# Optimization experiments

Hardware: AMD Instinct MI355X
Metric: run time of the kernel (lower is better)

The kernel has to match this reference:

```python
import jax, jax.numpy as jnp
import numpy as np
from jax import lax


def conv2d(x, w, b=None, pad=1):
    y = lax.conv_general_dilated(x, w, (1, 1), [(pad, pad), (pad, pad)],
                                 dimension_numbers=('NCHW', 'OIHW', 'NCHW'))
    return y if b is None else y + b[None, :, None, None]


def conv3d(x, w, b=None, pad=(0, 0, 0), dil=(1, 1, 1), groups=1):
    y = lax.conv_general_dilated(x, w, (1, 1, 1), [(p, p) for p in pad],
                                 rhs_dilation=dil,
                                 dimension_numbers=('NCDHW', 'OIDHW', 'NCDHW'),
                                 feature_group_count=groups)
    return y if b is None else y + b[None, :, None, None, None]


def base_grid(H, W, dtype):
    # normalized grid, channel 0 = x in [-1,1], channel 1 = y in [-1,1]
    gxn = 2.0 * jnp.arange(W, dtype=dtype) / max(W - 1, 1) - 1.0
    gyn = 2.0 * jnp.arange(H, dtype=dtype) / max(H - 1, 1) - 1.0
    return jnp.stack([jnp.broadcast_to(gxn[None, :], (H, W)),
                      jnp.broadcast_to(gyn[:, None], (H, W))], 0)


def grid_sample(img, grid):
    # img (N,C,H,W), grid (N,H,W,2) in [-1,1] (x,y); bilinear, zeros padding, align_corners=False
    N, C, H, W = img.shape
    gx = ((grid[..., 0] + 1.0) * W - 1.0) * 0.5
    gy = ((grid[..., 1] + 1.0) * H - 1.0) * 0.5
    x0 = jnp.floor(gx)
    y0 = jnp.floor(gy)
    wx = gx - x0
    wy = gy - y0

    def one(im, x0b, y0b, wxb, wyb):
        x0i = x0b.astype(jnp.int32)
        y0i = y0b.astype(jnp.int32)

        def samp(xi, yi):
            valid = (xi >= 0) & (xi < W) & (yi >= 0) & (yi < H)
            v = im[:, jnp.clip(yi, 0, H - 1), jnp.clip(xi, 0, W - 1)]
            return v * valid[None].astype(im.dtype)

        v00 = samp(x0i, y0i)
        v01 = samp(x0i + 1, y0i)
        v10 = samp(x0i, y0i + 1)
        v11 = samp(x0i + 1, y0i + 1)
        return (v00 * (1 - wxb) * (1 - wyb) + v01 * wxb * (1 - wyb)
                + v10 * (1 - wxb) * wyb + v11 * wxb * wyb)

    return jax.vmap(one)(img, x0, y0, wx, wy)


def ms_def_corr(x, y, off):
    # deformable correlation: per scale, warp y by that scale's offset and take
    # the channel-mean dot product with x -> (BT, S, H, W)
    BT, C, H, W = x.shape
    base = base_grid(H, W, x.dtype)
    sc = jnp.array([W - 1, H - 1], x.dtype)[None, :, None, None]
    S = off.shape[1] // 2
    corrs = []
    for i in range(S):
        vg = base[None] + off[:, 2 * i:2 * i + 2] / sc
        w = grid_sample(y, vg.transpose(0, 2, 3, 1))
        corrs.append(jnp.mean(x * w, axis=1))
    return jnp.stack(corrs, 1)


def corr_filter(corr, w1, w2):
    avg = jnp.mean(corr, 1, keepdims=True)
    mx = jnp.max(corr, 1, keepdims=True)
    var = jnp.var(corr, axis=1, keepdims=True, ddof=1)  # torch.var unbiased
    attn = jax.nn.sigmoid(conv2d(jnp.concatenate([avg, mx], 1), w1) + conv2d(var, w2))
    return corr * attn


def setup_inputs() -> dict:
    key = jax.random.key(0)
    ks = jax.random.split(key, 16)
    B, C, T, H, W = 2, 64, 16, 64, 64
    S = 3
    r = C // 16

    def n(k, shape, s=0.02):
        return jax.random.normal(k, shape, jnp.float32) * s

    return {
        'x': jax.random.normal(ks[0], (B, C, T, H, W), jnp.float32),
        'ofs_l_w1': n(ks[1], (C, 2 * C, 3, 3)), 'ofs_l_b1': jnp.zeros((C,), jnp.float32),
        'ofs_l_w2': n(ks[2], (2 * S, C, 3, 3)), 'ofs_l_b2': jnp.zeros((2 * S,), jnp.float32),
        'ofs_r_w1': n(ks[3], (C, 2 * C, 3, 3)), 'ofs_r_b1': jnp.zeros((C,), jnp.float32),
        'ofs_r_w2': n(ks[4], (2 * S, C, 3, 3)), 'ofs_r_b2': jnp.zeros((2 * S,), jnp.float32),
        'cf_w1': n(ks[5], (1, 2, 3, 3), 0.1), 'cf_w2': n(ks[6], (1, 1, 3, 3), 0.1),
        'down_w': n(ks[7], (r, C, 1, 1, 1), 0.1),
        'sa1_w': n(ks[8], (r, 1, 9, 3, 3), 0.1), 'sa1_b': jnp.zeros((r,), jnp.float32),
        'sa2_w': n(ks[9], (r, 1, 9, 3, 3), 0.1), 'sa2_b': jnp.zeros((r,), jnp.float32),
        'sa3_w': n(ks[10], (r, 1, 9, 3, 3), 0.1), 'sa3_b': jnp.zeros((r,), jnp.float32),
        'agg_w': jnp.ones((3,), jnp.float32) / 3,
        'back_w': n(ks[11], (C, r, 1, 1, 1), 0.1),
        'fusion_w': jnp.ones((2,), jnp.float32) / 2,
    }


def reference(x, ofs_l_w1, ofs_l_b1, ofs_l_w2, ofs_l_b2,
              ofs_r_w1, ofs_r_b1, ofs_r_w2, ofs_r_b2,
              cf_w1, cf_w2, down_w,
              sa1_w, sa1_b, sa2_w, sa2_b, sa3_w, sa3_b,
              agg_w, back_w, fusion_w):
    B, C, T, H, W = x.shape
    r = down_w.shape[0]

    # long-term branch: 1x1x1 down conv -> 3 dilated depthwise 3D convs -> 1x1x1 up conv
    x_agg = conv3d(x, down_w)
    agg = (conv3d(x_agg, sa1_w, sa1_b, (4, 1, 1), (1, 1, 1), r) * agg_w[0]
           + conv3d(x_agg, sa2_w, sa2_b, (4, 2, 2), (1, 2, 2), r) * agg_w[1]
           + conv3d(x_agg, sa3_w, sa3_b, (4, 3, 3), (1, 3, 3), r) * agg_w[2])
    long_term = jax.nn.sigmoid(conv3d(agg, back_w)) - 0.5

    # temporal shifts
    left = jnp.concatenate([x[:, :, 1:], x[:, :, -1:]], 2)
    right = jnp.concatenate([x[:, :, :1], x[:, :, :-1]], 2)
    xf = x.transpose(0, 2, 1, 3, 4).reshape(B * T, C, H, W)
    lf = left.transpose(0, 2, 1, 3, 4).reshape(B * T, C, H, W)
    rf = right.transpose(0, 2, 1, 3, 4).reshape(B * T, C, H, W)

    off_lm = conv2d(jax.nn.relu(conv2d(jnp.concatenate([xf, lf], 1), ofs_l_w1, ofs_l_b1)),
                    ofs_l_w2, ofs_l_b2)
    off_rm = conv2d(jax.nn.relu(conv2d(jnp.concatenate([xf, rf], 1), ofs_r_w1, ofs_r_b1)),
                    ofs_r_w2, ofs_r_b2)

    corr_lm = ms_def_corr(xf, lf, off_lm)
    corr_rm = ms_def_corr(xf, rf, off_rm)
    fcl = corr_filter(corr_lm, cf_w1, cf_w2)
    fcr = corr_filter(corr_rm, cf_w1, cf_w2)

    base = base_grid(H, W, x.dtype)
    sc = jnp.array([W - 1, H - 1], x.dtype)[None, :, None, None]
    vg_lm = base[None] + off_lm[:, :2] / sc
    vg_rm = base[None] + off_rm[:, :2] / sc
    warped_lm = grid_sample(lf, vg_lm.transpose(0, 2, 3, 1))
    warped_rm = grid_sample(rf, vg_rm.transpose(0, 2, 3, 1))

    attn_lm = jnp.mean(fcl, 1, keepdims=True)
    attn_rm = jnp.mean(fcr, 1, keepdims=True)
    feat_lm = warped_lm * (jax.nn.sigmoid(attn_lm) - 0.5)
    feat_rm = warped_rm * (jax.nn.sigmoid(attn_rm) - 0.5)

    short = fusion_w[0] * feat_lm + fusion_w[1] * feat_rm
    short = short.reshape(B, T, C, H, W).transpose(0, 2, 1, 3, 4)
    return short * long_term
```

## Files before the change

### kernel.cpp

```cpp
#include <hip/hip_runtime.h>
#include <hip/hip_bf16.h>
#include <math.h>


typedef __attribute__((ext_vector_type(8))) short short8v;
typedef __attribute__((ext_vector_type(4))) float f32x4;

#define HID_ELEMS 8650752ULL

__device__ __forceinline__ float sigmoidf_(float v) {
    return 1.0f / (1.0f + expf(-v));
}

__device__ __forceinline__ float bf2f(short s) {
    union { unsigned u; float f; } z;
    z.u = ((unsigned)(unsigned short)s) << 16;
    return z.f;
}

__device__ __forceinline__ void gll16(const __hip_bfloat16* g, __hip_bfloat16* l) {
    __builtin_amdgcn_global_load_lds((const __attribute__((address_space(1))) unsigned int*)(const void*)g,
                                     (__attribute__((address_space(3))) unsigned int*)(void*)l,
                                     16, 0, 0);
}

struct Samp { int o0, o1, o2, o3; float w0, w1, w2, w3; };

__device__ __forceinline__ Samp make_samp(float ox, float oy, int w, int h) {
    float bx = (2.0f * (float)w) / 63.0f - 1.0f;
    float by = (2.0f * (float)h) / 63.0f - 1.0f;
    float vx = bx + ox / 63.0f;
    float vy = by + oy / 63.0f;
    float gx = ((vx + 1.0f) * 64.0f - 1.0f) * 0.5f;
    float gy = ((vy + 1.0f) * 64.0f - 1.0f) * 0.5f;
    float fx = floorf(gx), fy = floorf(gy);
    float wx = gx - fx, wy = gy - fy;
    int x0 = (int)fx, y0 = (int)fy;
    int x1 = x0 + 1, y1 = y0 + 1;
    bool vx0 = (x0 >= 0) && (x0 < 64), vx1 = (x1 >= 0) && (x1 < 64);
    bool vy0 = (y0 >= 0) && (y0 < 64), vy1 = (y1 >= 0) && (y1 < 64);
    int cx0 = min(max(x0, 0), 63), cx1 = min(max(x1, 0), 63);
    int cy0 = min(max(y0, 0), 63), cy1 = min(max(y1, 0), 63);
    Samp s;
    s.o0 = cy0 * 4224 + (cx0 + 1) * 64; s.w0 = (1.0f - wx) * (1.0f - wy) * ((vx0 && vy0) ? 1.0f : 0.0f);
    s.o1 = cy0 * 4224 + (cx1 + 1) * 64; s.w1 = wx * (1.0f - wy) * ((vx1 && vy0) ? 1.0f : 0.0f);
    s.o2 = cy1 * 4224 + (cx0 + 1) * 64; s.w2 = (1.0f - wx) * wy * ((vx0 && vy1) ? 1.0f : 0.0f);
    s.o3 = cy1 * 4224 + (cx1 + 1) * 64; s.w3 = wx * wy * ((vx1 && vy1) ? 1.0f : 0.0f);
    return s;
}

__global__ __launch_bounds__(256) void k_prep_x(const float* __restrict__ x,
                                                const float* __restrict__ dw,
                                                __hip_bfloat16* __restrict__ xT,
                                                float* __restrict__ xa)
{
    int bid = blockIdx.x;
    int h = bid & 63;
    int n = bid >> 6;
    int b = n >> 4, t = n & 15;
    __shared__ float s[64][65];
    int tid = threadIdx.x;
    for (int idx = tid; idx < 4096; idx += 256) {
        int c = idx >> 6, w = idx & 63;
        s[c][w] = x[(((size_t)b * 64 + c) * 16 + t) * 4096 + h * 64 + w];
    }
    __syncthreads();
    __hip_bfloat16* op = xT + ((size_t)n * 64 + h) * 4224;
    for (int idx = tid; idx < 4224; idx += 256) {
        int wp = idx >> 6, c = idx & 63;
        float v = (wp == 0 || wp == 65) ? 0.f : s[c][wp - 1];
        op[idx] = __float2bfloat16(v);
    }
    int w = tid & 63, g = tid >> 6;
    float acc = 0.f;
    const float* dwg = dw + g * 64;
    #pragma unroll 8
    for (int c = 0; c < 64; c++) acc = fmaf(s[c][w], dwg[c], acc);
    xa[((size_t)(b * 4 + g) * 16 + t) * 4096 + h * 64 + w] = acc;
}

__global__ __launch_bounds__(256) void k_prep_w(const float* __restrict__ wl1,
                                                const float* __restrict__ wr1,
                                                const float* __restrict__ wl2,
                                                const float* __restrict__ wr2,
                                                __hip_bfloat16* __restrict__ Wmisc)
{
    int idx = blockIdx.x * 256 + threadIdx.x;
    if (idx < 147456) {
        int side = (idx >= 73728) ? 1 : 0;
        int i = idx - side * 73728;
        int ci = i & 127;
        int co = (i >> 7) & 63;
        int tap = i >> 13;
        const float* w = side ? wr1 : wl1;
        float v = w[((size_t)co * 128 + ci) * 9 + tap];
        int pos = side * 73728 + tap * 8192 + co * 128 + (ci ^ ((co & 15) << 3));
        Wmisc[pos] = __float2bfloat16(v);
    } else if (idx < 151680) {
        Wmisc[idx] = __float2bfloat16(0.f);
    } else if (idx < 170112) {
        int i2 = idx - 151680;
        int side = i2 / 9216;
        int j = i2 - side * 9216;
        int tap = j >> 10;
        int rem = j & 1023;
        int co = rem >> 6;
        int ci = rem & 63;
        const float* w = side ? wr2 : wl2;
        float v = (co < 6) ? w[((size_t)co * 64 + ci) * 9 + tap] : 0.f;
        Wmisc[idx] = __float2bfloat16(v);
    }
}

__global__ __launch_bounds__(512, 4) void k_conv1_mfma(const __hip_bfloat16* __restrict__ xT,
                                                       const __hip_bfloat16* __restrict__ Wb,
                                                       const __hip_bfloat16* __restrict__ zrow,
                                                       const float* __restrict__ b1l,
                                                       const float* __restrict__ b1r,
                                                       __hip_bfloat16* __restrict__ hidden,
                                                       int side_base, size_t hid_stride)
{
    __shared__ __hip_bfloat16 sB[24576];

    int bid = blockIdx.x;
    int side = side_base + (bid >> 9);
    int bid2 = bid & 511;
    int rq = bid2 & 15;
    int n = bid2 >> 4;
    int b = n >> 4, t = n & 15;
    int t2 = side ? max(t - 1, 0) : min(t + 1, 15);
    int n2 = b * 16 + t2;

    const __hip_bfloat16* WbS = Wb + (size_t)side * 73728;
    const float* b1 = side ? b1r : b1l;
    __hip_bfloat16* hs = hidden + (size_t)side * hid_stride;

    int tid = threadIdx.x;
    int wv = tid >> 6;
    int lane = tid & 63;
    int r = rq * 4 + (wv & 3);
    int m0 = (wv >> 2) * 32;
    int lr = lane & 15;
    int q = lane >> 4;
    int lk = q << 3;

    const __hip_bfloat16* fA0 = xT + (size_t)n * 270336;
    const __hip_bfloat16* fA1 = xT + (size_t)n2 * 270336;

    f32x4 acc[2][4];
    #pragma unroll
    for (int ni = 0; ni < 4; ni++) {
        float bb = b1[ni * 16 + lr];
        acc[0][ni] = (f32x4){bb, bb, bb, bb};
        acc[1][ni] = (f32x4){bb, bb, bb, bb};
    }

    int kx[2][2];
    #pragma unroll
    for (int khalf = 0; khalf < 2; khalf++)
        #pragma unroll
        for (int ks = 0; ks < 2; ks++)
            kx[khalf][ks] = ((khalf << 7) + (ks << 6) + (q << 4)) ^ (lr << 4);

    const char* sbc = (const char*)&sB[0];

    #pragma unroll
    for (int g = 0; g < 3; g++) {
        __syncthreads();
        {
            const __hip_bfloat16* wsrc = WbS + (size_t)g * 24576 + wv * 3072 + lane * 8;
            #pragma unroll
            for (int j = 0; j < 6; j++)
                gll16(wsrc + j * 512, &sB[wv * 3072 + j * 512]);
        }
        __syncthreads();

        int rr = r + g - 1;
        bool ok = (rr >= 0) && (rr < 64);
        const __hip_bfloat16* r0 = ok ? (fA0 + rr * 4224) : zrow;
        const __hip_bfloat16* r1 = ok ? (fA1 + rr * 4224) : zrow;

        #pragma unroll
        for (int tl = 0; tl < 3; tl++) {
            int abase = (m0 + lr + tl) * 64 + lk;
            #pragma unroll
            for (int khalf = 0; khalf < 2; khalf++) {
                const __hip_bfloat16* ar = khalf ? r1 : r0;
                short8v a00 = *(const short8v*)(ar + abase);
                short8v a01 = *(const short8v*)(ar + abase + 32);
                short8v a10 = *(const short8v*)(ar + abase + 1024);
                short8v a11 = *(const short8v*)(ar + abase + 1056);
                #pragma unroll
                for (int ni = 0; ni < 4; ni++) {
                    int rowb = tl * 16384 + ni * 4096 + lr * 256;
                    short8v b0  = *(const short8v*)(sbc + (rowb + kx[khalf][0]));
                    short8v b1v = *(const short8v*)(sbc + (rowb + kx[khalf][1]));
                    acc[0][ni] = __builtin_amdgcn_mfma_f32_16x16x32_bf16(a00, b0, acc[0][ni], 0, 0, 0);
                    acc[1][ni] = __builtin_amdgcn_mfma_f32_16x16x32_bf16(a10, b0, acc[1][ni], 0, 0, 0);
                    acc[0][ni] = __builtin_amdgcn_mfma_f32_16x16x32_bf16(a01, b1v, acc[0][ni], 0, 0, 0);
                    acc[1][ni] = __builtin_amdgcn_mfma_f32_16x16x32_bf16(a11, b1v, acc[1][ni], 0, 0, 0);
                }
            }
        }
    }

    int pxq = q << 2;
    __hip_bfloat16* hb = hs + (size_t)(n * 64 + r) * 4224;
    #pragma unroll
    for (int mi = 0; mi < 2; mi++) {
        #pragma unroll
        for (int ni = 0; ni < 4; ni++) {
            int co = ni * 16 + lr;
            #pragma unroll
            for (int j = 0; j < 4; j++) {
                int px = m0 + mi * 16 + pxq + j;
                float v = acc[mi][ni][j];
                v = v < 0.f ? 0.f : v;
                hb[(size_t)(px + 1) * 64 + co] = __float2bfloat16(v);
            }
        }
    }
    {
        int row_l = tid >> 7;
        int sel = (tid >> 6) & 1;
        int co = tid & 63;
        hs[(size_t)(n * 64 + rq * 4 + row_l) * 4224 + (sel ? 65 : 0) * 64 + co] = __float2bfloat16(0.f);
    }
}

__global__ __launch_bounds__(256) void k_conv2_mfma(const __hip_bfloat16* __restrict__ hidden,
                                                    const __hip_bfloat16* __restrict__ W2b,
                                                    const __hip_bfloat16* __restrict__ zrow,
                                                    const float* __restrict__ b2l,
                                                    const float* __restrict__ b2r,
                                                    float* __restrict__ off,
                                                    int side_base, size_t hid_stride)
{
    int bid = blockIdx.x;
    int side = side_base + (bid >> 9);
    int bid2 = bid & 511;
    int rq = bid2 & 15;
    int n = bid2 >> 4;
    int tid = threadIdx.x;
    int wv = tid >> 6;
    int lane = tid & 63;
    int r = rq * 4 + wv;
    int lr = lane & 15;
    int lk = (lane >> 4) << 3;

    const __hip_bfloat16* W2bS = W2b + (size_t)side * 9216;
    const float* b2 = side ? b2r : b2l;
    float* offS = off + (size_t)side * 786432;
    const __hip_bfloat16* hbase = hidden + (size_t)side * hid_stride + (size_t)n * 270336;

    float bb = (lr < 6) ? b2[lr] : 0.f;
    f32x4 acc[4];
    #pragma unroll
    for (int mi = 0; mi < 4; mi++) acc[mi] = (f32x4){bb, bb, bb, bb};

    #pragma unroll
    for (int tap = 0; tap < 9; tap++) {
        const int kh = tap / 3, kw = tap - (tap / 3) * 3;
        int rr = r + kh - 1;
        bool ok = (rr >= 0) && (rr < 64);
        const __hip_bfloat16* hr = ok ? (hbase + (size_t)rr * 4224) : zrow;
        const __hip_bfloat16* bw = W2bS + ((size_t)tap * 16 + lr) * 64 + lk;
        short8v b0 = *(const short8v*)(bw);
        short8v b1v = *(const short8v*)(bw + 32);
        #pragma unroll
        for (int mi = 0; mi < 4; mi++) {
            int abase = (mi * 16 + lr + kw) * 64 + lk;
            short8v a0 = *(const short8v*)(hr + abase);
            short8v a1 = *(const short8v*)(hr + abase + 32);
            acc[mi] = __builtin_amdgcn_mfma_f32_16x16x32_bf16(a0, b0, acc[mi], 0, 0, 0);
            acc[mi] = __builtin_amdgcn_mfma_f32_16x16x32_bf16(a1, b1v, acc[mi], 0, 0, 0);
        }
    }
    if (lr < 6) {
        int pxq = (lane >> 4) << 2;
        #pragma unroll
        for (int mi = 0; mi < 4; mi++) {
            #pragma unroll
            for (int j = 0; j < 4; j++) {
                int px = mi * 16 + pxq + j;
                offS[((size_t)n * 6 + lr) * 4096 + r * 64 + px] = acc[mi][j];
            }
        }
    }
}

__global__ __launch_bounds__(256) void k_agg(const float* __restrict__ xa,
                                             const float* __restrict__ w1, const float* __restrict__ b1,
                                             const float* __restrict__ w2, const float* __restrict__ b2,
                                             const float* __restrict__ w3, const float* __restrict__ b3,
                                             const float* __restrict__ aw,
                                             float* __restrict__ agg)
{
    int gid = blockIdx.x * 256 + threadIdx.x;
    int hw = gid & 4095;
    int rest = gid >> 12;
    int t = rest & 15;
    int g = (rest >> 4) & 3;
    int b = rest >> 6;
    int h = hw >> 6, w = hw & 63;
    const float* base = xa + ((size_t)(b * 4 + g) * 16) * 4096;
    const float* ws0 = w1 + g * 81;
    const float* ws1 = w2 + g * 81;
    const float* ws2 = w3 + g * 81;
    float acc0 = b1[g], acc1 = b2[g], acc2 = b3[g];
    for (int kd = 0; kd < 9; kd++) {
        int d = t + kd - 4;
        if (d < 0 || d > 15) continue;
        const float* fr = base + (size_t)d * 4096;
        #pragma unroll
        for (int kh = 0; kh < 3; kh++) {
            #pragma unroll
            for (int kw = 0; kw < 3; kw++) {
                int widx = kd * 9 + kh * 3 + kw;
                {
                    int yy = h + (kh - 1), xx = w + (kw - 1);
                    if (yy >= 0 && yy < 64 && xx >= 0 && xx < 64)
                        acc0 = fmaf(fr[yy * 64 + xx], ws0[widx], acc0);
                }
                {
                    int yy = h + (kh - 1) * 2, xx = w + (kw - 1) * 2;
                    if (yy >= 0 && yy < 64 && xx >= 0 && xx < 64)
                        acc1 = fmaf(fr[yy * 64 + xx], ws1[widx], acc1);
                }
                {
                    int yy = h + (kh - 1) * 3, xx = w + (kw - 1) * 3;
                    if (yy >= 0 && yy < 64 && xx >= 0 && xx < 64)
                        acc2 = fmaf(fr[yy * 64 + xx], ws2[widx], acc2);
                }
            }
        }
    }
    agg[gid] = acc0 * aw[0] + acc1 * aw[1] + acc2 * aw[2];
}

__global__ __launch_bounds__(256, 4) void k_corr2(const __hip_bfloat16* __restrict__ xT,
                                                  const float* __restrict__ off_l,
                                                  const float* __restrict__ off_r,
                                                  float* __restrict__ stats_l,
                                                  float* __restrict__ stats_r)
{
    int tid = threadIdx.x;
    int wv = tid >> 6;
    int lane = tid & 63;
    int pl = lane & 15;
    int cq = lane >> 4;
    int pidx = blockIdx.x * 64 + wv * 16 + pl;
    int half = pidx >> 17;
    int gid = pidx & 131071;
    const float* off = half ? off_r : off_l;
    float* stats = half ? stats_r : stats_l;

    int hw = gid & 4095;
    int n = gid >> 12;
    int b = n >> 4, t = n & 15;
    int t2 = half ? max(t - 1, 0) : min(t + 1, 15);
    int n2 = b * 16 + t2;
    int h = hw >> 6, w = hw & 63;
    int cc0 = cq * 16;

    const __hip_bfloat16* xf = xT + (size_t)n * 270336 + h * 4224 + (w + 1) * 64 + cc0;
    const __hip_bfloat16* yf = xT + (size_t)n2 * 270336 + cc0;

    Samp sp[3];
    #pragma unroll
    for (int s = 0; s < 3; s++) {
        float ox = off[((size_t)n * 6 + 2 * s) * 4096 + hw];
        float oy = off[((size_t)n * 6 + 2 * s + 1) * 4096 + hw];
        sp[s] = make_samp(ox, oy, w, h);
    }

    short8v xv0 = *(const short8v*)(xf);
    short8v xv1 = *(const short8v*)(xf + 8);

    int o0[4] = {sp[0].o0, sp[0].o1, sp[0].o2, sp[0].o3};
    int o1[4] = {sp[1].o0, sp[1].o1, sp[1].o2, sp[1].o3};
    int o2[4] = {sp[2].o0, sp[2].o1, sp[2].o2, sp[2].o3};

    short8v y0[4][2], y1[4][2], y2[4][2];
    #pragma unroll
    for (int cr = 0; cr < 4; cr++) {
        y0[cr][0] = *(const short8v*)(yf + o0[cr]);
        y0[cr][1] = *(const short8v*)(yf + o0[cr] + 8);
    }
    #pragma unroll
    for (int cr = 0; cr < 4; cr++) {
        y1[cr][0] = *(const short8v*)(yf + o1[cr]);
        y1[cr][1] = *(const short8v*)(yf + o1[cr] + 8);
    }

    float xs[16];
    #pragma unroll
    for (int e = 0; e < 8; e++) { xs[e] = bf2f(xv0[e]); xs[8 + e] = bf2f(xv1[e]); }

    float ac[3][4];
    #pragma unroll
    for (int s = 0; s < 3; s++)
        #pragma unroll
        for (int cr = 0; cr < 4; cr++) ac[s][cr] = 0.f;

    #pragma unroll
    for (int cr = 0; cr < 4; cr++)
        #pragma unroll
        for (int i = 0; i < 2; i++)
            #pragma unroll
            for (int e = 0; e < 8; e++)
                ac[0][cr] = fmaf(xs[i * 8 + e], bf2f(y0[cr][i][e]), ac[0][cr]);
    #pragma unroll
    for (int cr = 0; cr < 4; cr++) {
        y2[cr][0] = *(const short8v*)(yf + o2[cr]);
        y2[cr][1] = *(const short8v*)(yf + o2[cr] + 8);
    }
    #pragma unroll
    for (int cr = 0; cr < 4; cr++)
        #pragma unroll
        for (int i = 0; i < 2; i++)
            #pragma unroll
            for (int e = 0; e < 8; e++)
                ac[1][cr] = fmaf(xs[i * 8 + e], bf2f(y1[cr][i][e]), ac[1][cr]);
    #pragma unroll
    for (int cr = 0; cr < 4; cr++)
        #pragma unroll
        for (int i = 0; i < 2; i++)
            #pragma unroll
            for (int e = 0; e < 8; e++)
                ac[2][cr] = fmaf(xs[i * 8 + e], bf2f(y2[cr][i][e]), ac[2][cr]);

    #pragma unroll
    for (int s = 0; s < 3; s++)
        #pragma unroll
        for (int cr = 0; cr < 4; cr++) {
            float v = ac[s][cr];
            v += __shfl_xor(v, 16, 64);
            v += __shfl_xor(v, 32, 64);
            ac[s][cr] = v;
        }

    if (cq == 0) {
        float c[3];
        c[0] = (ac[0][0] * sp[0].w0 + ac[0][1] * sp[0].w1 + ac[0][2] * sp[0].w2 + ac[0][3] * sp[0].w3) * (1.0f / 64.0f);
        c[1] = (ac[1][0] * sp[1].w0 + ac[1][1] * sp[1].w1 + ac[1][2] * sp[1].w2 + ac[1][3] * sp[1].w3) * (1.0f / 64.0f);
        c[2] = (ac[2][0] * sp[2].w0 + ac[2][1] * sp[2].w1 + ac[2][2] * sp[2].w2 + ac[2][3] * sp[2].w3) * (1.0f / 64.0f);
        float avg = (c[0] + c[1] + c[2]) * (1.0f / 3.0f);
        float mx = fmaxf(c[0], fmaxf(c[1], c[2]));
        float d0 = c[0] - avg, d1 = c[1] - avg, d2 = c[2] - avg;
        float var = (d0 * d0 + d1 * d1 + d2 * d2) * 0.5f;
        stats[(size_t)n * 4096 + hw] = avg;
        stats[131072 + (size_t)n * 4096 + hw] = mx;
        stats[262144 + (size_t)n * 4096 + hw] = var;
    }
}

__device__ __forceinline__ float attn_val(const float* __restrict__ stats, int n, int hw,
                                          const float* __restrict__ cfw1,
                                          const float* __restrict__ cfw2)
{
    int h = hw >> 6, w = hw & 63;
    const float* avg = stats + (size_t)n * 4096;
    const float* mx  = stats + 131072 + (size_t)n * 4096;
    const float* var = stats + 262144 + (size_t)n * 4096;
    float s = 0.f;
    #pragma unroll
    for (int k = 0; k < 9; k++) {
        int kh = k / 3 - 1, kw = k - (k / 3) * 3 - 1;
        int yy = h + kh, xx = w + kw;
        if (yy >= 0 && yy < 64 && xx >= 0 && xx < 64) {
            int p = yy * 64 + xx;
            s += avg[p] * cfw1[k] + mx[p] * cfw1[9 + k] + var[p] * cfw2[k];
        }
    }
    float attn = sigmoidf_(s);
    return sigmoidf_(avg[hw] * attn) - 0.5f;
}

__global__ __launch_bounds__(256) void k_final(const __hip_bfloat16* __restrict__ xT,
                                               const float* __restrict__ off_l,
                                               const float* __restrict__ off_r,
                                               const float* __restrict__ stats_l,
                                               const float* __restrict__ stats_r,
                                               const float* __restrict__ cfw1,
                                               const float* __restrict__ cfw2,
                                               const float* __restrict__ agg,
                                               const float* __restrict__ backw,
                                               const float* __restrict__ fusw,
                                               float* __restrict__ out)
{
    int gid0 = blockIdx.x * 256 + threadIdx.x;
    int hw = gid0 & 4095;
    int ch = (gid0 >> 12) & 1;
    int n = gid0 >> 13;
    int b = n >> 4, t = n & 15;
    int tl = min(t + 1, 15), tr = max(t - 1, 0);
    int nl = b * 16 + tl, nr = b * 16 + tr;
    int h = hw >> 6, w = hw & 63;
    int cc0 = ch * 32;

    float oxl = off_l[((size_t)n * 6 + 0) * 4096 + hw];
    float oyl = off_l[((size_t)n * 6 + 1) * 4096 + hw];
    float oxr = off_r[((size_t)n * 6 + 0) * 4096 + hw];
    float oyr = off_r[((size_t)n * 6 + 1) * 4096 + hw];
    Samp sl = make_samp(oxl, oyl, w, h);
    Samp sr = make_samp(oxr, oyr, w, h);

    const __hip_bfloat16* lf = xT + (size_t)nl * 270336 + cc0;
    const __hip_bfloat16* rf = xT + (size_t)nr * 270336 + cc0;

    short8v lv[4][4], rv[4][4];
    #pragma unroll
    for (int i = 0; i < 4; i++) {
        lv[0][i] = *(const short8v*)(lf + sl.o0 + 8 * i);
        lv[1][i] = *(const short8v*)(lf + sl.o1 + 8 * i);
        lv[2][i] = *(const short8v*)(lf + sl.o2 + 8 * i);
        lv[3][i] = *(const short8v*)(lf + sl.o3 + 8 * i);
        rv[0][i] = *(const short8v*)(rf + sr.o0 + 8 * i);
        rv[1][i] = *(const short8v*)(rf + sr.o1 + 8 * i);
        rv[2][i] = *(const short8v*)(rf + sr.o2 + 8 * i);
        rv[3][i] = *(const short8v*)(rf + sr.o3 + 8 * i);
    }

    float Al = attn_val(stats_l, n, hw, cfw1, cfw2) * fusw[0];
    float Ar = attn_val(stats_r, n, hw, cfw1, cfw2) * fusw[1];

    float ag0 = agg[((size_t)(b * 4 + 0) * 16 + t) * 4096 + hw];
    float ag1 = agg[((size_t)(b * 4 + 1) * 16 + t) * 4096 + hw];
    float ag2 = agg[((size_t)(b * 4 + 2) * 16 + t) * 4096 + hw];
    float ag3 = agg[((size_t)(b * 4 + 3) * 16 + t) * 4096 + hw];

    #pragma unroll
    for (int i = 0; i < 4; i++) {
        #pragma unroll
        for (int e = 0; e < 8; e++) {
            int c = cc0 + i * 8 + e;
            float wl = sl.w0 * bf2f(lv[0][i][e]) + sl.w1 * bf2f(lv[1][i][e])
                     + sl.w2 * bf2f(lv[2][i][e]) + sl.w3 * bf2f(lv[3][i][e]);
            float wr = sr.w0 * bf2f(rv[0][i][e]) + sr.w1 * bf2f(rv[1][i][e])
                     + sr.w2 * bf2f(rv[2][i][e]) + sr.w3 * bf2f(rv[3][i][e]);
            float lt = sigmoidf_(ag0 * backw[c * 4 + 0] + ag1 * backw[c * 4 + 1]
                               + ag2 * backw[c * 4 + 2] + ag3 * backw[c * 4 + 3]) - 0.5f;
            out[(((size_t)b * 64 + c) * 16 + t) * 4096 + hw] = (wl * Al + wr * Ar) * lt;
        }
    }
}

extern "C" void kernel_launch(void* const* d_in, const int* in_sizes, int n_in,
                              void* d_out, int out_size, void* d_ws, size_t ws_size,
                              hipStream_t stream)
{
    const float* x     = (const float*)d_in[0];
    const float* lw1   = (const float*)d_in[1];
    const float* lb1   = (const float*)d_in[2];
    const float* lw2   = (const float*)d_in[3];
    const float* lb2   = (const float*)d_in[4];
    const float* rw1   = (const float*)d_in[5];
    const float* rb1   = (const float*)d_in[6];
    const float* rw2   = (const float*)d_in[7];
    const float* rb2   = (const float*)d_in[8];
    const float* cfw1  = (const float*)d_in[9];
    const float* cfw2  = (const float*)d_in[10];
    const float* downw = (const float*)d_in[11];
    const float* sa1w  = (const float*)d_in[12];
    const float* sa1b  = (const float*)d_in[13];
    const float* sa2w  = (const float*)d_in[14];
    const float* sa2b  = (const float*)d_in[15];
    const float* sa3w  = (const float*)d_in[16];
    const float* sa3b  = (const float*)d_in[17];
    const float* aggw  = (const float*)d_in[18];
    const float* backw = (const float*)d_in[19];
    const float* fusw  = (const float*)d_in[20];
    float* out = (float*)d_out;

    float* ws      = (float*)d_ws;
    float* x_agg   = ws;
    float* agg     = x_agg + 524288;
    float* off_l   = agg + 524288;
    float* off_r   = off_l + 786432;
    float* stats_l = off_r + 786432;
    float* stats_r = stats_l + 393216;
    __hip_bfloat16* hidden  = (__hip_bfloat16*)(stats_r + 393216);
    __hip_bfloat16* xT      = hidden + HID_ELEMS;
    __hip_bfloat16* Wmisc   = xT + HID_ELEMS;
    __hip_bfloat16* Wb      = Wmisc;
    __hip_bfloat16* zrow    = Wmisc + 147456;
    __hip_bfloat16* W2bL    = Wmisc + 151680;
    __hip_bfloat16* hidden2 = Wmisc + 170112;

    const size_t need_merged = 65876224ULL;
    const bool merged = (ws_size >= need_merged);
    const size_t hid_stride = merged ? (size_t)(hidden2 - hidden) : 0;

    k_prep_x<<<2048, 256, 0, stream>>>(x, downw, xT, x_agg);
    k_prep_w<<<665, 256, 0, stream>>>(lw1, rw1, lw2, rw2, Wmisc);

    k_agg<<<2048, 256, 0, stream>>>(x_agg, sa1w, sa1b, sa2w, sa2b, sa3w, sa3b, aggw, agg);

    if (merged) {
        k_conv1_mfma<<<1024, 512, 0, stream>>>(xT, Wb, zrow, lb1, rb1, hidden, 0, hid_stride);
        k_conv2_mfma<<<1024, 256, 0, stream>>>(hidden, W2bL, zrow, lb2, rb2, off_l, 0, hid_stride);
    } else {
        k_conv1_mfma<<<512, 512, 0, stream>>>(xT, Wb, zrow, lb1, rb1, hidden, 0, 0);
        k_conv2_mfma<<<512, 256, 0, stream>>>(hidden, W2bL, zrow, lb2, rb2, off_l, 0, 0);
        k_conv1_mfma<<<512, 512, 0, stream>>>(xT, Wb, zrow, lb1, rb1, hidden, 1, 0);
        k_conv2_mfma<<<512, 256, 0, stream>>>(hidden, W2bL, zrow, lb2, rb2, off_l, 1, 0);
    }

    k_corr2<<<4096, 256, 0, stream>>>(xT, off_l, off_r, stats_l, stats_r);

    k_final<<<1024, 256, 0, stream>>>(xT, off_l, off_r, stats_l, stats_r, cfw1, cfw2,
                                      agg, backw, fusw, out);
}
```

Before: 259.3 us.

## Switch conv1 to 32x32x16 MFMA with whole-row per-wave tiles

Rewrites the first offset-conv kernel to use 32x32x16 bf16 MFMA instructions instead of 16x16x32. Each wave now computes a full 64-pixel row for all 64 output channels, and each block covers 8 rows instead of 4, which halves the grid. The intent is to reload the staged weight tile from LDS fewer times per block and to issue fewer, larger MFMAs. In exchange each thread holds more accumulator registers, the grid is smaller so occupancy may drop, and the epilogue stores are more scattered.

```diff
diff --git a/kernel.cpp b/kernel.cpp
--- a/kernel.cpp
+++ b/kernel.cpp
@@ -5,6 +5,7 @@
 
 typedef __attribute__((ext_vector_type(8))) short short8v;
 typedef __attribute__((ext_vector_type(4))) float f32x4;
+typedef __attribute__((ext_vector_type(16))) float f32x16;
 
 #define HID_ELEMS 8650752ULL
 
@@ -123,10 +124,10 @@
     __shared__ __hip_bfloat16 sB[24576];
 
     int bid = blockIdx.x;
-    int side = side_base + (bid >> 9);
-    int bid2 = bid & 511;
-    int rq = bid2 & 15;
-    int n = bid2 >> 4;
+    int side = side_base + (bid >> 8);
+    int bid2 = bid & 255;
+    int rq = bid2 & 7;
+    int n = bid2 >> 3;
     int b = n >> 4, t = n & 15;
     int t2 = side ? max(t - 1, 0) : min(t + 1, 15);
     int n2 = b * 16 + t2;
@@ -138,93 +139,92 @@
     int tid = threadIdx.x;
     int wv = tid >> 6;
     int lane = tid & 63;
-    int r = rq * 4 + (wv & 3);
-    int m0 = (wv >> 2) * 32;
-    int lr = lane & 15;
-    int q = lane >> 4;
-    int lk = q << 3;
+    int r = rq * 8 + wv;
+    int l31 = lane & 31;
+    int lh = lane >> 5;
 
     const __hip_bfloat16* fA0 = xT + (size_t)n * 270336;
     const __hip_bfloat16* fA1 = xT + (size_t)n2 * 270336;
 
-    f32x4 acc[2][4];
-    #pragma unroll
-    for (int ni = 0; ni < 4; ni++) {
-        float bb = b1[ni * 16 + lr];
-        acc[0][ni] = (f32x4){bb, bb, bb, bb};
-        acc[1][ni] = (f32x4){bb, bb, bb, bb};
-    }
-
-    int kx[2][2];
-    #pragma unroll
-    for (int khalf = 0; khalf < 2; khalf++)
-        #pragma unroll
-        for (int ks = 0; ks < 2; ks++)
-            kx[khalf][ks] = ((khalf << 7) + (ks << 6) + (q << 4)) ^ (lr << 4);
+    f32x16 acc[2][2];
+    #pragma unroll
+    for (int ni = 0; ni < 2; ni++) {
+        float bb = b1[ni * 32 + l31];
+        #pragma unroll
+        for (int mi = 0; mi < 2; mi++)
+            #pragma unroll
+            for (int j = 0; j < 16; j++) acc[mi][ni][j] = bb;
+    }
 
     const char* sbc = (const char*)&sB[0];
+    int xr = l31 & 15;
 
     #pragma unroll
     for (int g = 0; g < 3; g++) {
-        __syncthreads();
-        {
-            const __hip_bfloat16* wsrc = WbS + (size_t)g * 24576 + wv * 3072 + lane * 8;
-            #pragma unroll
-            for (int j = 0; j < 6; j++)
-                gll16(wsrc + j * 512, &sB[wv * 3072 + j * 512]);
-        }
-        __syncthreads();
-
         int rr = r + g - 1;
         bool ok = (rr >= 0) && (rr < 64);
         const __hip_bfloat16* r0 = ok ? (fA0 + rr * 4224) : zrow;
         const __hip_bfloat16* r1 = ok ? (fA1 + rr * 4224) : zrow;
 
+        __syncthreads();
+        {
+            const __hip_bfloat16* wsrc = WbS + (size_t)g * 24576 + wv * 3072 + lane * 8;
+            #pragma unroll
+            for (int j = 0; j < 6; j++)
+                gll16(wsrc + j * 512, &sB[wv * 3072 + j * 512]);
+        }
+        __syncthreads();
+
         #pragma unroll
         for (int tl = 0; tl < 3; tl++) {
-            int abase = (m0 + lr + tl) * 64 + lk;
+            int abase = (l31 + tl) * 64 + lh * 8;
             #pragma unroll
             for (int khalf = 0; khalf < 2; khalf++) {
                 const __hip_bfloat16* ar = khalf ? r1 : r0;
-                short8v a00 = *(const short8v*)(ar + abase);
-                short8v a01 = *(const short8v*)(ar + abase + 32);
-                short8v a10 = *(const short8v*)(ar + abase + 1024);
-                short8v a11 = *(const short8v*)(ar + abase + 1056);
+                short8v a[2][4];
                 #pragma unroll
-                for (int ni = 0; ni < 4; ni++) {
-                    int rowb = tl * 16384 + ni * 4096 + lr * 256;
-                    short8v b0  = *(const short8v*)(sbc + (rowb + kx[khalf][0]));
-                    short8v b1v = *(const short8v*)(sbc + (rowb + kx[khalf][1]));
-                    acc[0][ni] = __builtin_amdgcn_mfma_f32_16x16x32_bf16(a00, b0, acc[0][ni], 0, 0, 0);
-                    acc[1][ni] = __builtin_amdgcn_mfma_f32_16x16x32_bf16(a10, b0, acc[1][ni], 0, 0, 0);
-                    acc[0][ni] = __builtin_amdgcn_mfma_f32_16x16x32_bf16(a01, b1v, acc[0][ni], 0, 0, 0);
-                    acc[1][ni] = __builtin_amdgcn_mfma_f32_16x16x32_bf16(a11, b1v, acc[1][ni], 0, 0, 0);
+                for (int mi = 0; mi < 2; mi++)
+                    #pragma unroll
+                    for (int kk = 0; kk < 4; kk++)
+                        a[mi][kk] = *(const short8v*)(ar + abase + mi * 2048 + kk * 16);
+                #pragma unroll
+                for (int kk = 0; kk < 4; kk++) {
+                    int slot = khalf * 8 + kk * 2 + lh;
+                    int soff = (slot ^ xr) << 4;
+                    #pragma unroll
+                    for (int ni = 0; ni < 2; ni++) {
+                        int baddr = tl * 16384 + (ni * 32 + l31) * 256 + soff;
+                        short8v bf = *(const short8v*)(sbc + baddr);
+                        acc[0][ni] = __builtin_amdgcn_mfma_f32_32x32x16_bf16(a[0][kk], bf, acc[0][ni], 0, 0, 0);
+                        acc[1][ni] = __builtin_amdgcn_mfma_f32_32x32x16_bf16(a[1][kk], bf, acc[1][ni], 0, 0, 0);
+                    }
                 }
             }
         }
     }
 
-    int pxq = q << 2;
     __hip_bfloat16* hb = hs + (size_t)(n * 64 + r) * 4224;
     #pragma unroll
     for (int mi = 0; mi < 2; mi++) {
         #pragma unroll
-        for (int ni = 0; ni < 4; ni++) {
-            int co = ni * 16 + lr;
-            #pragma unroll
-            for (int j = 0; j < 4; j++) {
-                int px = m0 + mi * 16 + pxq + j;
+        for (int ni = 0; ni < 2; ni++) {
+            int co = ni * 32 + l31;
+            #pragma unroll
+            for (int j = 0; j < 16; j++) {
+                int px = mi * 32 + (j & 3) + 8 * (j >> 2) + 4 * lh;
                 float v = acc[mi][ni][j];
                 v = v < 0.f ? 0.f : v;
                 hb[(size_t)(px + 1) * 64 + co] = __float2bfloat16(v);
             }
         }
     }
-    {
-        int row_l = tid >> 7;
-        int sel = (tid >> 6) & 1;
-        int co = tid & 63;
-        hs[(size_t)(n * 64 + rq * 4 + row_l) * 4224 + (sel ? 65 : 0) * 64 + co] = __float2bfloat16(0.f);
+    #pragma unroll
+    for (int z = 0; z < 2; z++) {
+        int idx = z * 512 + tid;
+        int co = idx & 63;
+        int sel = (idx >> 6) & 1;
+        int row_l = idx >> 7;
+        hs[(size_t)(n * 64 + rq * 8 + row_l) * 4224 + (sel ? 65 : 0) * 64 + co] = __float2bfloat16(0.f);
     }
 }
 
@@ -598,12 +598,12 @@
     k_agg<<<2048, 256, 0, stream>>>(x_agg, sa1w, sa1b, sa2w, sa2b, sa3w, sa3b, aggw, agg);
 
     if (merged) {
-        k_conv1_mfma<<<1024, 512, 0, stream>>>(xT, Wb, zrow, lb1, rb1, hidden, 0, hid_stride);
+        k_conv1_mfma<<<512, 512, 0, stream>>>(xT, Wb, zrow, lb1, rb1, hidden, 0, hid_stride);
         k_conv2_mfma<<<1024, 256, 0, stream>>>(hidden, W2bL, zrow, lb2, rb2, off_l, 0, hid_stride);
     } else {
-        k_conv1_mfma<<<512, 512, 0, stream>>>(xT, Wb, zrow, lb1, rb1, hidden, 0, 0);
+        k_conv1_mfma<<<256, 512, 0, stream>>>(xT, Wb, zrow, lb1, rb1, hidden, 0, 0);
         k_conv2_mfma<<<512, 256, 0, stream>>>(hidden, W2bL, zrow, lb2, rb2, off_l, 0, 0);
-        k_conv1_mfma<<<512, 512, 0, stream>>>(xT, Wb, zrow, lb1, rb1, hidden, 1, 0);
+        k_conv1_mfma<<<256, 512, 0, stream>>>(xT, Wb, zrow, lb1, rb1, hidden, 1, 0);
         k_conv2_mfma<<<512, 256, 0, stream>>>(hidden, W2bL, zrow, lb2, rb2, off_l, 1, 0);
     }
 
```

Result: slower. 265.7 us (+2.5%).
